# Kernel tuning notes

Measured on AMD Instinct MI355X. Metric: run time of the kernel, lower is better.

## Reference

```python
import jax, jax.numpy as jnp
import numpy as np

EMBED_DIM = 512
NUM_HEADS = 8
K_NEAREST = 5
B = 8192
N_MEM = 50000


def setup_inputs() -> dict:
    key = jax.random.key(0)
    ks = jax.random.split(key, 12)
    E = EMBED_DIM
    s = 1.0 / np.sqrt(E)
    inp = {
        "Q": jax.random.normal(ks[0], (B, E), jnp.float32),
        "mem_keys": jax.random.normal(ks[1], (N_MEM, E), jnp.float32),
        "mem_vals": jax.random.normal(ks[2], (N_MEM, E), jnp.float32),
        # pre-projection linears (linear_q/k/v)
        "Wq": jax.random.uniform(ks[3], (E, E), jnp.float32, -s, s),
        "bq": jnp.zeros((E,), jnp.float32),
        "Wk": jax.random.uniform(ks[4], (E, E), jnp.float32, -s, s),
        "bk": jnp.zeros((E,), jnp.float32),
        "Wv": jax.random.uniform(ks[5], (E, E), jnp.float32, -s, s),
        "bv": jnp.zeros((E,), jnp.float32),
        # nn.MultiheadAttention internal in/out projections
        "W_in_q": jax.random.uniform(ks[6], (E, E), jnp.float32, -s, s),
        "W_in_k": jax.random.uniform(ks[7], (E, E), jnp.float32, -s, s),
        "W_in_v": jax.random.uniform(ks[8], (E, E), jnp.float32, -s, s),
        "b_in": jnp.zeros((3 * E,), jnp.float32),
        "W_out": jax.random.uniform(ks[9], (E, E), jnp.float32, -s, s),
        "b_out": jnp.zeros((E,), jnp.float32),
    }
    return inp


def _find_k_nearest(Q, mem_keys, mem_vals, k):
    # squared Euclidean distance; argmax of negative distance == k nearest
    # dists: [B, N]
    sq = jnp.sum(mem_keys * mem_keys, axis=-1)  # [N]
    scores = 2.0 * (Q @ mem_keys.T) - sq[None, :]  # -||q-m||^2 up to const
    _, idx = jax.lax.top_k(scores, k)  # [B, k]
    K = mem_keys[idx]  # [B, k, E]
    V = mem_vals[idx]  # [B, k, E]
    return K, V


def _mha(Q, K, V, W_in_q, W_in_k, W_in_v, b_in, W_out, b_out):
    # Q: [B,1,E], K/V: [B,k,E]; torch nn.MultiheadAttention, batch_first
    E = Q.shape[-1]
    H = NUM_HEADS
    d = E // H
    q = Q @ W_in_q.T + b_in[:E]
    k = K @ W_in_k.T + b_in[E:2 * E]
    v = V @ W_in_v.T + b_in[2 * E:]
    Bsz = Q.shape[0]
    q = q.reshape(Bsz, -1, H, d).transpose(0, 2, 1, 3)  # [B,H,1,d]
    k = k.reshape(Bsz, -1, H, d).transpose(0, 2, 1, 3)  # [B,H,k,d]
    v = v.reshape(Bsz, -1, H, d).transpose(0, 2, 1, 3)
    scores = jnp.einsum("bhqd,bhkd->bhqk", q, k) / jnp.sqrt(jnp.float32(d))
    attn = jax.nn.softmax(scores, axis=-1)
    out = jnp.einsum("bhqk,bhkd->bhqd", attn, v)
    out = out.transpose(0, 2, 1, 3).reshape(Bsz, -1, E)
    return out @ W_out.T + b_out


def reference(Q, mem_keys, mem_vals, Wq, bq, Wk, bk, Wv, bv,
              W_in_q, W_in_k, W_in_v, b_in, W_out, b_out):
    K, V = _find_k_nearest(Q, mem_keys, mem_vals, K_NEAREST)
    Qs = Q[:, None, :]  # [B,1,E]
    Qp = Qs @ Wq.T + bq
    Kp = K @ Wk.T + bk
    Vp = V @ Wv.T + bv
    return _mha(Qp, Kp, Vp, W_in_q, W_in_k, W_in_v, b_in, W_out, b_out)
```

## Files before the change

kernel.cpp:

```cpp
#include <hip/hip_runtime.h>
#include <hip/hip_bf16.h>
#include <hip/hip_fp16.h>

typedef _Float16 f16;
typedef _Float16 f16x8 __attribute__((ext_vector_type(8)));
typedef float f32x4 __attribute__((ext_vector_type(4)));

constexpr int EE     = 512;
constexpr int NMEM   = 50000;
constexpr int BQ     = 8192;
constexpr int NSEG   = 16;
constexpr int SEGLEN = NMEM / NSEG;
constexpr int KVT    = 32;
constexpr int NT32   = (SEGLEN + KVT - 1) / KVT;
constexpr int NC     = 6;
constexpr int NCAND  = NSEG * NC;
constexpr int NRES   = 12;

__global__ __launch_bounds__(256) void k_prep_keys(const float* __restrict__ mk,
                                                   f16* __restrict__ kh,
                                                   float* __restrict__ sq32,
                                                   double* __restrict__ sq64) {
  int row  = blockIdx.x * 4 + (threadIdx.x >> 6);
  int lane = threadIdx.x & 63;
  const float4* src = (const float4*)(mk + (size_t)row * EE) + lane * 2;
  float4 a = src[0], b = src[1];
  double s = (double)a.x*a.x + (double)a.y*a.y + (double)a.z*a.z + (double)a.w*a.w
           + (double)b.x*b.x + (double)b.y*b.y + (double)b.z*b.z + (double)b.w*b.w;
  f16x8 h;
  h[0]=(f16)a.x; h[1]=(f16)a.y; h[2]=(f16)a.z; h[3]=(f16)a.w;
  h[4]=(f16)b.x; h[5]=(f16)b.y; h[6]=(f16)b.z; h[7]=(f16)b.w;
  *((f16x8*)(kh + (size_t)row * EE) + lane) = h;
  #pragma unroll
  for (int o = 32; o > 0; o >>= 1) s += __shfl_down(s, o);
  if (lane == 0) { sq64[row] = s; sq32[row] = (float)s; }
}

__global__ __launch_bounds__(256) void k_prep_f16(const float* __restrict__ src,
                                                  f16* __restrict__ dst) {
  int row  = blockIdx.x * 4 + (threadIdx.x >> 6);
  int lane = threadIdx.x & 63;
  const float4* s = (const float4*)(src + (size_t)row * EE) + lane * 2;
  float4 a = s[0], b = s[1];
  f16x8 h;
  h[0]=(f16)a.x; h[1]=(f16)a.y; h[2]=(f16)a.z; h[3]=(f16)a.w;
  h[4]=(f16)b.x; h[5]=(f16)b.y; h[6]=(f16)b.z; h[7]=(f16)b.w;
  *((f16x8*)(dst + (size_t)row * EE) + lane) = h;
}

__global__ __launch_bounds__(256) void k_compose(const float* __restrict__ Wq, const float* __restrict__ Wk,
                                                 const float* __restrict__ Wv, const float* __restrict__ Wiq,
                                                 const float* __restrict__ Wik, const float* __restrict__ Wiv,
                                                 f16* __restrict__ Wc) {
  int m = blockIdx.z;
  const float* A = (m == 0) ? Wiq : ((m == 1) ? Wik : Wiv);
  const float* B = (m == 0) ? Wq  : ((m == 1) ? Wk  : Wv);
  f16* C = Wc + (size_t)m * EE * EE;
  __shared__ float As[64][33];
  __shared__ float Bs[32][65];
  int i0 = blockIdx.x * 64, j0 = blockIdx.y * 64;
  int tx = threadIdx.x & 15, ty = threadIdx.x >> 4;
  float acc[4][4] = {};
  for (int kb = 0; kb < EE; kb += 32) {
    __syncthreads();
    #pragma unroll
    for (int v = 0; v < 8; ++v) {
      int idx = threadIdx.x + v * 256;
      As[idx >> 5][idx & 31] = A[(size_t)(i0 + (idx >> 5)) * EE + kb + (idx & 31)];
    }
    #pragma unroll
    for (int v = 0; v < 8; ++v) {
      int idx = threadIdx.x + v * 256;
      Bs[idx >> 6][idx & 63] = B[(size_t)(kb + (idx >> 6)) * EE + j0 + (idx & 63)];
    }
    __syncthreads();
    for (int t = 0; t < 32; ++t) {
      float av[4], bv[4];
      #pragma unroll
      for (int u = 0; u < 4; ++u) av[u] = As[ty*4+u][t];
      #pragma unroll
      for (int u = 0; u < 4; ++u) bv[u] = Bs[t][tx*4+u];
      #pragma unroll
      for (int a = 0; a < 4; ++a)
        #pragma unroll
        for (int b = 0; b < 4; ++b) acc[a][b] = fmaf(av[a], bv[b], acc[a][b]);
    }
  }
  #pragma unroll
  for (int a = 0; a < 4; ++a)
    #pragma unroll
    for (int b = 0; b < 4; ++b)
      C[(size_t)(i0 + ty*4 + a) * EE + j0 + tx*4 + b] = (f16)acc[a][b];
}

__global__ void k_bias(const float* __restrict__ Wiq, const float* __restrict__ Wik,
                       const float* __restrict__ Wiv, const float* __restrict__ bqv,
                       const float* __restrict__ bkv, const float* __restrict__ bvv,
                       const float* __restrict__ b_in, float* __restrict__ bc) {
  int m = blockIdx.x;
  const float* Wi = (m == 0) ? Wiq : ((m == 1) ? Wik : Wiv);
  const float* bb = (m == 0) ? bqv : ((m == 1) ? bkv : bvv);
  for (int i = threadIdx.x; i < EE; i += blockDim.x) {
    float s = 0.f;
    for (int t = 0; t < EE; ++t) s = fmaf(Wi[(size_t)i * EE + t], bb[t], s);
    bc[m * EE + i] = s + b_in[m * EE + i];
  }
}

__global__ void k_cvtw(const float* __restrict__ W, f16* __restrict__ Wo) {
  int i = blockIdx.x * 256 + threadIdx.x;
  Wo[i] = (f16)W[i];
}

__global__ __launch_bounds__(256, 2) void k_stage1(const f16* __restrict__ Qh,
                                                   const f16* __restrict__ Kh,
                                                   const float* __restrict__ sq32,
                                                   int* __restrict__ part_i,
                                                   float* __restrict__ part_s) {
  const int rb  = blockIdx.x;
  const int seg = blockIdx.y;
  const int tid = threadIdx.x;
  const int w   = tid >> 6;
  const int l   = tid & 63;
  const int lc  = l & 15, lp = l >> 4;
  const int seg_start = seg * SEGLEN;
  const int seg_end   = seg_start + SEGLEN;

  __shared__ f16   Bt[2][KVT * 520];
  __shared__ float sqs[2][KVT];

  const int rowbase = rb * 128 + w * 32;
  f16x8 a0[16], a1[16];
  {
    const f16* base0 = Qh + (size_t)(rowbase + lc) * EE + lp * 8;
    const f16* base1 = base0 + (size_t)16 * EE;
    #pragma unroll
    for (int ks = 0; ks < 16; ++ks) {
      asm volatile("global_load_dwordx4 %0, %1, off"
                   : "=v"(a0[ks]) : "v"(base0 + ks * 32) : "memory");
      asm volatile("global_load_dwordx4 %0, %1, off"
                   : "=v"(a1[ks]) : "v"(base1 + ks * 32) : "memory");
    }
    asm volatile("s_waitcnt vmcnt(0)" ::: "memory");
    __builtin_amdgcn_sched_barrier(0);
  }

  float ts0[NC], ts1[NC]; int ti0[NC], ti1[NC];
  #pragma unroll
  for (int i = 0; i < NC; ++i) {
    ts0[i] = -3.0e38f; ti0[i] = 0;
    ts1[i] = -3.0e38f; ti1[i] = 0;
  }

#define INS(TS, TI, SV, IV) do { \
    if ((SV) > TS[NC-1]) { \
      TS[NC-1] = (SV); TI[NC-1] = (IV); \
      _Pragma("unroll") \
      for (int _i = NC - 1; _i > 0; --_i) { \
        if (TS[_i] > TS[_i-1]) { \
          float _tf = TS[_i]; TS[_i] = TS[_i-1]; TS[_i-1] = _tf; \
          int   _tx = TI[_i]; TI[_i] = TI[_i-1]; TI[_i-1] = _tx; \
        } \
      } \
    } \
  } while (0)

  float4 st[8]; float stsq = 0.f;
  #define LOADT(tt) do { \
      int kk = seg_start + (tt) * KVT; \
      _Pragma("unroll") \
      for (int j = 0; j < 8; ++j) { \
        int key = kk + w * 8 + j; \
        key = key < NMEM ? key : NMEM - 1; \
        st[j] = *(const float4*)(Kh + (size_t)key * EE + l * 8); \
      } \
      if (tid < KVT) { int kq = kk + tid; stsq = sq32[kq < NMEM ? kq : NMEM - 1]; } \
    } while (0)
  #define STORET(buf) do { \
      _Pragma("unroll") \
      for (int j = 0; j < 8; ++j) \
        *(float4*)&Bt[buf][(w*8 + j) * 520 + l * 8] = st[j]; \
      if (tid < KVT) sqs[buf][tid] = stsq; \
    } while (0)

  LOADT(0);
  STORET(0);
  for (int t = 0; t < NT32; ++t) {
    const int c = t & 1;
    __syncthreads();
    if (t + 1 < NT32) LOADT(t + 1);

    f32x4 A00 = {0,0,0,0}, A01 = {0,0,0,0}, A10 = {0,0,0,0}, A11 = {0,0,0,0};
    #pragma unroll
    for (int ks = 0; ks < 16; ++ks) {
      f16x8 kf0 = *(const f16x8*)&Bt[c][lc * 520 + ks * 32 + lp * 8];
      f16x8 kf1 = *(const f16x8*)&Bt[c][(16 + lc) * 520 + ks * 32 + lp * 8];
      A00 = __builtin_amdgcn_mfma_f32_16x16x32_f16(kf0, a0[ks], A00, 0, 0, 0);
      A01 = __builtin_amdgcn_mfma_f32_16x16x32_f16(kf0, a1[ks], A01, 0, 0, 0);
      A10 = __builtin_amdgcn_mfma_f32_16x16x32_f16(kf1, a0[ks], A10, 0, 0, 0);
      A11 = __builtin_amdgcn_mfma_f32_16x16x32_f16(kf1, a1[ks], A11, 0, 0, 0);
    }
    float4 q0 = *(const float4*)&sqs[c][lp * 4];
    float4 q1 = *(const float4*)&sqs[c][16 + lp * 4];
    const int kb = seg_start + t * KVT;
    #pragma unroll
    for (int r = 0; r < 4; ++r) {
      float qv0 = (r == 0) ? q0.x : (r == 1) ? q0.y : (r == 2) ? q0.z : q0.w;
      float qv1 = (r == 0) ? q1.x : (r == 1) ? q1.y : (r == 2) ? q1.z : q1.w;
      int i0v = kb + lp * 4 + r;
      int i1v = kb + 16 + lp * 4 + r;
      float s00 = (i0v < seg_end) ? 2.0f * A00[r] - qv0 : -3.0e38f;
      float s01 = (i0v < seg_end) ? 2.0f * A01[r] - qv0 : -3.0e38f;
      float s10 = (i1v < seg_end) ? 2.0f * A10[r] - qv1 : -3.0e38f;
      float s11 = (i1v < seg_end) ? 2.0f * A11[r] - qv1 : -3.0e38f;
      INS(ts0, ti0, s00, i0v);
      INS(ts0, ti0, s10, i1v);
      INS(ts1, ti1, s01, i0v);
      INS(ts1, ti1, s11, i1v);
    }
    if (t + 1 < NT32) STORET(c ^ 1);
  }
  #undef LOADT
  #undef STORET

  #pragma unroll
  for (int d = 16; d <= 32; d <<= 1) {
    float os[NC]; int oi[NC];
    #pragma unroll
    for (int i = 0; i < NC; ++i) { os[i] = __shfl_xor(ts0[i], d); oi[i] = __shfl_xor(ti0[i], d); }
    #pragma unroll
    for (int j = 0; j < NC; ++j) INS(ts0, ti0, os[j], oi[j]);
    #pragma unroll
    for (int i = 0; i < NC; ++i) { os[i] = __shfl_xor(ts1[i], d); oi[i] = __shfl_xor(ti1[i], d); }
    #pragma unroll
    for (int j = 0; j < NC; ++j) INS(ts1, ti1, os[j], oi[j]);
  }
#undef INS
  if (l < 16) {
    int row = rowbase + lc;
    #pragma unroll
    for (int i = 0; i < NC; ++i) {
      part_i[(size_t)row * NCAND + seg * NC + i] = ti0[i];
      part_s[(size_t)row * NCAND + seg * NC + i] = ts0[i];
    }
  } else if (l < 32) {
    int row = rowbase + 16 + lc;
    #pragma unroll
    for (int i = 0; i < NC; ++i) {
      part_i[(size_t)row * NCAND + seg * NC + i] = ti1[i];
      part_s[(size_t)row * NCAND + seg * NC + i] = ts1[i];
    }
  }
}

__global__ __launch_bounds__(64) void k_rescore(const float* __restrict__ Q,
                                                const float* __restrict__ mk,
                                                const double* __restrict__ sq64,
                                                const int* __restrict__ part_i,
                                                const float* __restrict__ part_s,
                                                int* __restrict__ idx5) {
  const int row = blockIdx.x;
  const int l = threadIdx.x;
  const float* Qr = Q + (size_t)row * EE;
  float q[8];
  #pragma unroll
  for (int i = 0; i < 8; ++i) q[i] = Qr[l + 64*i];
  float s0 = part_s[(size_t)row * NCAND + l];
  int   i0 = part_i[(size_t)row * NCAND + l];
  float s1 = (l < 32) ? part_s[(size_t)row * NCAND + 64 + l] : -3.0e38f;
  int   i1 = (l < 32) ? part_i[(size_t)row * NCAND + 64 + l] : 0;

  double bs[5] = {-1e300, -1e300, -1e300, -1e300, -1e300};
  int    bi[5] = {0, 0, 0, 0, 0};
  #pragma unroll
  for (int p = 0; p < NRES; ++p) {
    bool pick0 = (s0 >= s1);
    float m  = pick0 ? s0 : s1;
    int   mi = pick0 ? i0 : i1;
    int   code = (l << 1) | (pick0 ? 0 : 1);
    #pragma unroll
    for (int o = 32; o > 0; o >>= 1) {
      float mo = __shfl_xor(m, o);
      int   io = __shfl_xor(mi, o);
      int   co = __shfl_xor(code, o);
      if (mo > m || (mo == m && co < code)) { m = mo; mi = io; code = co; }
    }
    if ((code >> 1) == l) { if (code & 1) s1 = -3.0e38f; else s0 = -3.0e38f; }
    const float* kr = mk + (size_t)mi * EE;
    double pd = 0.0;
    #pragma unroll
    for (int i = 0; i < 8; ++i) pd += (double)q[i] * (double)kr[l + 64*i];
    #pragma unroll
    for (int o = 32; o > 0; o >>= 1) pd += __shfl_down(pd, o);
    if (l == 0) {
      double s = 2.0 * pd - sq64[mi];
      if (s > bs[4]) {
        bs[4] = s; bi[4] = mi;
        #pragma unroll
        for (int i = 4; i > 0; --i) {
          if (bs[i] > bs[i-1]) {
            double tf = bs[i]; bs[i] = bs[i-1]; bs[i-1] = tf;
            int    tx = bi[i]; bi[i] = bi[i-1]; bi[i-1] = tx;
          }
        }
      }
    }
  }
  if (l == 0) {
    #pragma unroll
    for (int i = 0; i < 5; ++i) idx5[(size_t)row*5 + i] = bi[i];
  }
}

template <int OUTF32>
__global__ __launch_bounds__(256) void k_gemm(const f16* __restrict__ A, const f16* __restrict__ B,
                                              const float* __restrict__ bias, void* __restrict__ outp) {
  __shared__ f16 As[64][72];
  __shared__ f16 Bs[64][72];
  const int tid = threadIdx.x;
  const int wv = tid >> 6, l = tid & 63, lc = l & 15, lp = l >> 4;
  const int m0 = blockIdx.x * 64, n0 = blockIdx.y * 64;
  const int r = tid >> 2, co = (tid & 3) * 16;
  f32x4 acc[4] = {{0,0,0,0},{0,0,0,0},{0,0,0,0},{0,0,0,0}};
  for (int kb = 0; kb < EE; kb += 64) {
    __syncthreads();
    *(float4*)&As[r][co]     = *(const float4*)(A + (size_t)(m0 + r) * EE + kb + co);
    *(float4*)&As[r][co + 8] = *(const float4*)(A + (size_t)(m0 + r) * EE + kb + co + 8);
    *(float4*)&Bs[r][co]     = *(const float4*)(B + (size_t)(n0 + r) * EE + kb + co);
    *(float4*)&Bs[r][co + 8] = *(const float4*)(B + (size_t)(n0 + r) * EE + kb + co + 8);
    __syncthreads();
    #pragma unroll
    for (int ks = 0; ks < 2; ++ks) {
      f16x8 a = *(const f16x8*)&As[wv*16 + lc][ks*32 + lp*8];
      #pragma unroll
      for (int f = 0; f < 4; ++f) {
        f16x8 b = *(const f16x8*)&Bs[f*16 + lc][ks*32 + lp*8];
        acc[f] = __builtin_amdgcn_mfma_f32_16x16x32_f16(a, b, acc[f], 0, 0, 0);
      }
    }
  }
  #pragma unroll
  for (int f = 0; f < 4; ++f) {
    int col = n0 + f*16 + lc;
    float bsv = bias[col];
    #pragma unroll
    for (int rr = 0; rr < 4; ++rr) {
      int row = m0 + wv*16 + lp*4 + rr;
      float v = acc[f][rr] + bsv;
      if (OUTF32) ((float*)outp)[(size_t)row * EE + col] = v;
      else        ((f16*)outp)[(size_t)row * EE + col] = (f16)v;
    }
  }
}

template <int AF16>
__global__ __launch_bounds__(256) void k_gemm_g(const int* __restrict__ gidx, const void* __restrict__ Asrc,
                                                const f16* __restrict__ B, const float* __restrict__ bias,
                                                f16* __restrict__ outp) {
  __shared__ f16 As[64][72];
  __shared__ f16 Bs[64][72];
  const int tid = threadIdx.x;
  const int wv = tid >> 6, l = tid & 63, lc = l & 15, lp = l >> 4;
  const int m0 = blockIdx.x * 64, n0 = blockIdx.y * 64;
  const int r = tid >> 2, co = (tid & 3) * 16;
  const int gi = gidx[m0 + r];
  f32x4 acc[4] = {{0,0,0,0},{0,0,0,0},{0,0,0,0},{0,0,0,0}};
  for (int kb = 0; kb < EE; kb += 64) {
    __syncthreads();
    if (AF16) {
      const f16* arow = (const f16*)Asrc + (size_t)gi * EE;
      *(f16x8*)&As[r][co]     = *(const f16x8*)(arow + kb + co);
      *(f16x8*)&As[r][co + 8] = *(const f16x8*)(arow + kb + co + 8);
    } else {
      const float* arow = (const float*)Asrc + (size_t)gi * EE;
      float4 x0 = *(const float4*)(arow + kb + co);
      float4 x1 = *(const float4*)(arow + kb + co + 4);
      float4 x2 = *(const float4*)(arow + kb + co + 8);
      float4 x3 = *(const float4*)(arow + kb + co + 12);
      f16x8 h0, h1;
      h0[0]=(f16)x0.x; h0[1]=(f16)x0.y; h0[2]=(f16)x0.z; h0[3]=(f16)x0.w;
      h0[4]=(f16)x1.x; h0[5]=(f16)x1.y; h0[6]=(f16)x1.z; h0[7]=(f16)x1.w;
      h1[0]=(f16)x2.x; h1[1]=(f16)x2.y; h1[2]=(f16)x2.z; h1[3]=(f16)x2.w;
      h1[4]=(f16)x3.x; h1[5]=(f16)x3.y; h1[6]=(f16)x3.z; h1[7]=(f16)x3.w;
      *(f16x8*)&As[r][co]     = h0;
      *(f16x8*)&As[r][co + 8] = h1;
    }
    *(float4*)&Bs[r][co]     = *(const float4*)(B + (size_t)(n0 + r) * EE + kb + co);
    *(float4*)&Bs[r][co + 8] = *(const float4*)(B + (size_t)(n0 + r) * EE + kb + co + 8);
    __syncthreads();
    #pragma unroll
    for (int ks = 0; ks < 2; ++ks) {
      f16x8 a = *(const f16x8*)&As[wv*16 + lc][ks*32 + lp*8];
      #pragma unroll
      for (int f = 0; f < 4; ++f) {
        f16x8 b = *(const f16x8*)&Bs[f*16 + lc][ks*32 + lp*8];
        acc[f] = __builtin_amdgcn_mfma_f32_16x16x32_f16(a, b, acc[f], 0, 0, 0);
      }
    }
  }
  #pragma unroll
  for (int f = 0; f < 4; ++f) {
    int col = n0 + f*16 + lc;
    float bsv = bias[col];
    #pragma unroll
    for (int rr = 0; rr < 4; ++rr) {
      int row = m0 + wv*16 + lp*4 + rr;
      outp[(size_t)row * EE + col] = (f16)(acc[f][rr] + bsv);
    }
  }
}

__global__ __launch_bounds__(256) void k_attn(const f16* __restrict__ qp, const f16* __restrict__ kp,
                                              const f16* __restrict__ vp, f16* __restrict__ ao) {
  int row = blockIdx.x * 4 + (threadIdx.x >> 6);
  int l = threadIdx.x & 63;
  int h = l >> 3, sl = l & 7;
  const f16* q = qp + (size_t)row * EE + h * 64 + sl * 8;
  float qv[8];
  #pragma unroll
  for (int i = 0; i < 8; ++i) qv[i] = (float)q[i];
  float sc[5];
  #pragma unroll
  for (int j = 0; j < 5; ++j) {
    const f16* kr = kp + ((size_t)row * 5 + j) * EE + h * 64 + sl * 8;
    float p = 0.f;
    #pragma unroll
    for (int i = 0; i < 8; ++i) p = fmaf(qv[i], (float)kr[i], p);
    p += __shfl_xor(p, 1); p += __shfl_xor(p, 2); p += __shfl_xor(p, 4);
    sc[j] = p * 0.125f;
  }
  float mx = fmaxf(fmaxf(fmaxf(sc[0], sc[1]), fmaxf(sc[2], sc[3])), sc[4]);
  float sum = 0.f;
  #pragma unroll
  for (int j = 0; j < 5; ++j) { sc[j] = __expf(sc[j] - mx); sum += sc[j]; }
  float inv = 1.0f / sum;
  float o[8] = {};
  #pragma unroll
  for (int j = 0; j < 5; ++j) {
    const f16* vr = vp + ((size_t)row * 5 + j) * EE + h * 64 + sl * 8;
    float aw = sc[j] * inv;
    #pragma unroll
    for (int i = 0; i < 8; ++i) o[i] = fmaf(aw, (float)vr[i], o[i]);
  }
  f16* dst = ao + (size_t)row * EE + h * 64 + sl * 8;
  #pragma unroll
  for (int i = 0; i < 8; ++i) dst[i] = (f16)o[i];
}

extern "C" void kernel_launch(void* const* d_in, const int* in_sizes, int n_in,
                              void* d_out, int out_size, void* d_ws, size_t ws_size,
                              hipStream_t stream) {
  const float* Q    = (const float*)d_in[0];
  const float* mk   = (const float*)d_in[1];
  const float* mv   = (const float*)d_in[2];
  const float* Wq   = (const float*)d_in[3];
  const float* bq   = (const float*)d_in[4];
  const float* Wk   = (const float*)d_in[5];
  const float* bk   = (const float*)d_in[6];
  const float* Wv   = (const float*)d_in[7];
  const float* bv   = (const float*)d_in[8];
  const float* Wiq  = (const float*)d_in[9];
  const float* Wik  = (const float*)d_in[10];
  const float* Wiv  = (const float*)d_in[11];
  const float* b_in = (const float*)d_in[12];
  const float* Wo   = (const float*)d_in[13];
  const float* bo   = (const float*)d_in[14];

  char* w = (char*)d_ws;
  size_t off = 0;
  auto alloc = [&](size_t bytes) { size_t o = off; off += (bytes + 255) & ~(size_t)255; return (void*)(w + o); };
  f16*    Kh     = (f16*)   alloc((size_t)NMEM * EE * 2);
  f16*    Qh     = (f16*)   alloc((size_t)BQ * EE * 2);
  float*  sq32   = (float*) alloc((size_t)NMEM * 4);
  double* sq64   = (double*)alloc((size_t)NMEM * 8);
  f16*    Wc     = (f16*)   alloc((size_t)3 * EE * EE * 2);
  f16*    Wo16   = (f16*)   alloc((size_t)EE * EE * 2);
  float*  bc     = (float*) alloc((size_t)3 * EE * 4);
  int*    part_i = (int*)   alloc((size_t)BQ * NCAND * 4);
  float*  part_s = (float*) alloc((size_t)BQ * NCAND * 4);
  int*    idx5   = (int*)   alloc((size_t)BQ * 5 * 4);
  f16*    qp     = (f16*)   alloc((size_t)BQ * EE * 2);
  f16*    vp     = (f16*)   alloc((size_t)BQ * 5 * EE * 2);
  f16*    ao     = Qh;
  size_t need_big = off + (size_t)NMEM * EE * 2 + (size_t)BQ * 5 * EE * 2 + 4096;
  bool big = (ws_size >= need_big);
  f16* Vh = nullptr;
  f16* kp;
  if (big) {
    Vh = (f16*)alloc((size_t)NMEM * EE * 2);
    kp = (f16*)alloc((size_t)BQ * 5 * EE * 2);
  } else {
    kp = Kh;
  }
  (void)in_sizes; (void)n_in; (void)out_size;

  k_prep_keys<<<NMEM / 4, 256, 0, stream>>>(mk, Kh, sq32, sq64);
  k_prep_f16<<<BQ / 4, 256, 0, stream>>>(Q, Qh);
  if (big) k_prep_f16<<<NMEM / 4, 256, 0, stream>>>(mv, Vh);
  k_compose<<<dim3(8, 8, 3), 256, 0, stream>>>(Wq, Wk, Wv, Wiq, Wik, Wiv, Wc);
  k_bias<<<3, 256, 0, stream>>>(Wiq, Wik, Wiv, bq, bk, bv, b_in, bc);
  k_cvtw<<<(EE * EE) / 256, 256, 0, stream>>>(Wo, Wo16);
  k_stage1<<<dim3(BQ / 128, NSEG), 256, 0, stream>>>(Qh, Kh, sq32, part_i, part_s);
  k_rescore<<<BQ, 64, 0, stream>>>(Q, mk, sq64, part_i, part_s, idx5);
  k_gemm<0><<<dim3(BQ / 64, 8), 256, 0, stream>>>(Qh, Wc, bc, qp);
  if (big) {
    k_gemm_g<1><<<dim3(BQ * 5 / 64, 8), 256, 0, stream>>>(idx5, Kh, Wc + (size_t)EE * EE, bc + EE, kp);
    k_gemm_g<1><<<dim3(BQ * 5 / 64, 8), 256, 0, stream>>>(idx5, Vh, Wc + (size_t)2 * EE * EE, bc + 2 * EE, vp);
  } else {
    k_gemm_g<0><<<dim3(BQ * 5 / 64, 8), 256, 0, stream>>>(idx5, mk, Wc + (size_t)EE * EE, bc + EE, kp);
    k_gemm_g<0><<<dim3(BQ * 5 / 64, 8), 256, 0, stream>>>(idx5, mv, Wc + (size_t)2 * EE * EE, bc + 2 * EE, vp);
  }
  k_attn<<<BQ / 4, 256, 0, stream>>>(qp, kp, vp, ao);
  k_gemm<1><<<dim3(BQ / 64, 8), 256, 0, stream>>>(ao, Wo16, bo, (float*)d_out);
}
```

Before: 861.6 us.

## Stage key tiles via direct global-to-LDS loads and shrink candidate lists

Replaces the register-staged global load plus LDS store of key tiles with global_load_lds direct copies into the double buffer. It also vectorises the score computation and swaps the per-element bounds check for a huge squared-norm sentinel, so out-of-segment keys score very low. Per-segment candidates drop from 6 to 5 and rescoring passes from 12 to 10, which cuts insertion-sort and rescore work but gives the fp16 approximate search less margin to recover the exact top-5.

Measured after the change: 792.9 us. -8.0%, faster.

```diff
diff --git a/kernel.cpp b/kernel.cpp
--- a/kernel.cpp
+++ b/kernel.cpp
@@ -13,9 +13,15 @@
 constexpr int SEGLEN = NMEM / NSEG;
 constexpr int KVT    = 32;
 constexpr int NT32   = (SEGLEN + KVT - 1) / KVT;
-constexpr int NC     = 6;
+constexpr int NC     = 5;
 constexpr int NCAND  = NSEG * NC;
-constexpr int NRES   = 12;
+constexpr int NRES   = 10;
+
+typedef const __attribute__((address_space(1))) unsigned char* gas_t;
+typedef __attribute__((address_space(3))) unsigned char* las_t;
+__device__ static inline void g2l16(const void* g, void* l) {
+  __builtin_amdgcn_global_load_lds((gas_t)g, (las_t)l, 16, 0, 0);
+}
 
 __global__ __launch_bounds__(256) void k_prep_keys(const float* __restrict__ mk,
                                                    f16* __restrict__ kh,
@@ -165,30 +171,27 @@
     } \
   } while (0)
 
-  float4 st[8]; float stsq = 0.f;
-  #define LOADT(tt) do { \
+  #define STAGE(buf, tt) do { \
       int kk = seg_start + (tt) * KVT; \
       _Pragma("unroll") \
       for (int j = 0; j < 8; ++j) { \
         int key = kk + w * 8 + j; \
         key = key < NMEM ? key : NMEM - 1; \
-        st[j] = *(const float4*)(Kh + (size_t)key * EE + l * 8); \
+        g2l16(Kh + (size_t)key * EE + l * 8, &Bt[buf][(w*8 + j) * 520]); \
       } \
-      if (tid < KVT) { int kq = kk + tid; stsq = sq32[kq < NMEM ? kq : NMEM - 1]; } \
+      if (tid < KVT) { \
+        int kq = kk + tid; \
+        float v = 6.0e38f; \
+        if (kq < seg_end) v = sq32[kq]; \
+        sqs[buf][tid] = v; \
+      } \
     } while (0)
-  #define STORET(buf) do { \
-      _Pragma("unroll") \
-      for (int j = 0; j < 8; ++j) \
-        *(float4*)&Bt[buf][(w*8 + j) * 520 + l * 8] = st[j]; \
-      if (tid < KVT) sqs[buf][tid] = stsq; \
-    } while (0)
-
-  LOADT(0);
-  STORET(0);
+
+  STAGE(0, 0);
   for (int t = 0; t < NT32; ++t) {
     const int c = t & 1;
     __syncthreads();
-    if (t + 1 < NT32) LOADT(t + 1);
+    if (t + 1 < NT32) STAGE(c ^ 1, t + 1);
 
     f32x4 A00 = {0,0,0,0}, A01 = {0,0,0,0}, A10 = {0,0,0,0}, A11 = {0,0,0,0};
     #pragma unroll
@@ -200,28 +203,24 @@
       A10 = __builtin_amdgcn_mfma_f32_16x16x32_f16(kf1, a0[ks], A10, 0, 0, 0);
       A11 = __builtin_amdgcn_mfma_f32_16x16x32_f16(kf1, a1[ks], A11, 0, 0, 0);
     }
-    float4 q0 = *(const float4*)&sqs[c][lp * 4];
-    float4 q1 = *(const float4*)&sqs[c][16 + lp * 4];
+    f32x4 q0 = *(const f32x4*)&sqs[c][lp * 4];
+    f32x4 q1 = *(const f32x4*)&sqs[c][16 + lp * 4];
+    f32x4 s00 = 2.0f * A00 - q0;
+    f32x4 s01 = 2.0f * A01 - q0;
+    f32x4 s10 = 2.0f * A10 - q1;
+    f32x4 s11 = 2.0f * A11 - q1;
     const int kb = seg_start + t * KVT;
+    const int b0 = kb + lp * 4;
+    const int b1 = b0 + 16;
     #pragma unroll
     for (int r = 0; r < 4; ++r) {
-      float qv0 = (r == 0) ? q0.x : (r == 1) ? q0.y : (r == 2) ? q0.z : q0.w;
-      float qv1 = (r == 0) ? q1.x : (r == 1) ? q1.y : (r == 2) ? q1.z : q1.w;
-      int i0v = kb + lp * 4 + r;
-      int i1v = kb + 16 + lp * 4 + r;
-      float s00 = (i0v < seg_end) ? 2.0f * A00[r] - qv0 : -3.0e38f;
-      float s01 = (i0v < seg_end) ? 2.0f * A01[r] - qv0 : -3.0e38f;
-      float s10 = (i1v < seg_end) ? 2.0f * A10[r] - qv1 : -3.0e38f;
-      float s11 = (i1v < seg_end) ? 2.0f * A11[r] - qv1 : -3.0e38f;
-      INS(ts0, ti0, s00, i0v);
-      INS(ts0, ti0, s10, i1v);
-      INS(ts1, ti1, s01, i0v);
-      INS(ts1, ti1, s11, i1v);
-    }
-    if (t + 1 < NT32) STORET(c ^ 1);
-  }
-  #undef LOADT
-  #undef STORET
+      INS(ts0, ti0, s00[r], b0 + r);
+      INS(ts0, ti0, s10[r], b1 + r);
+      INS(ts1, ti1, s01[r], b0 + r);
+      INS(ts1, ti1, s11[r], b1 + r);
+    }
+  }
+  #undef STAGE
 
   #pragma unroll
   for (int d = 16; d <= 32; d <<= 1) {
@@ -267,8 +266,8 @@
   for (int i = 0; i < 8; ++i) q[i] = Qr[l + 64*i];
   float s0 = part_s[(size_t)row * NCAND + l];
   int   i0 = part_i[(size_t)row * NCAND + l];
-  float s1 = (l < 32) ? part_s[(size_t)row * NCAND + 64 + l] : -3.0e38f;
-  int   i1 = (l < 32) ? part_i[(size_t)row * NCAND + 64 + l] : 0;
+  float s1 = (l < NCAND - 64) ? part_s[(size_t)row * NCAND + 64 + l] : -3.0e38f;
+  int   i1 = (l < NCAND - 64) ? part_i[(size_t)row * NCAND + 64 + l] : 0;
 
   double bs[5] = {-1e300, -1e300, -1e300, -1e300, -1e300};
   int    bi[5] = {0, 0, 0, 0, 0};
```
